# Optimization experiments

Measured on AMD Instinct MI355X. Metric: run time of the kernel, lower is better.

## Reference

```python
import jax, jax.numpy as jnp
import numpy as np
import math

B, N, C = 16, 4096, 256
WS = 8            # window_size
NH = 8            # num_heads
HD = C // NH      # head_dim = 32
LK = 32           # linformer compressed length
G = 16            # global bank tokens


def setup_inputs() -> dict:
    key = jax.random.key(0)
    ks = jax.random.split(key, 10)
    x = jax.random.normal(ks[0], (B, N, C), dtype=jnp.float32)
    W_qkv = jax.random.normal(ks[1], (C, 3 * C), dtype=jnp.float32) * 0.02
    b_qkv = jnp.zeros((3 * C,), dtype=jnp.float32)
    E_k = jax.random.normal(ks[2], (WS * WS, LK), dtype=jnp.float32) * 0.02
    E_v = jax.random.normal(ks[3], (WS * WS, LK), dtype=jnp.float32) * 0.02
    k_bank = jax.random.normal(ks[4], (G, C), dtype=jnp.float32)
    v_bank = jax.random.normal(ks[5], (G, C), dtype=jnp.float32)
    W_proj = jax.random.normal(ks[6], (C, C), dtype=jnp.float32) * 0.02
    b_proj = jnp.zeros((C,), dtype=jnp.float32)
    return {"x": x, "W_qkv": W_qkv, "b_qkv": b_qkv, "E_k": E_k, "E_v": E_v,
            "k_bank": k_bank, "v_bank": v_bank, "W_proj": W_proj, "b_proj": b_proj,
            "window_size": WS, "num_heads": NH}


def reference(x, W_qkv, b_qkv, E_k, E_v, k_bank, v_bank, W_proj, b_proj, window_size, num_heads):
    Bb, Nn, Cc = x.shape
    Hs = int(math.isqrt(Nn))          # H = W = sqrt(N), divisible by window_size here
    ws = window_size
    nh = Hs // ws                      # windows per side
    hd = Cc // num_heads
    NW = ws * ws                       # tokens per window

    # ---- window partition: [B,N,C] -> [BW, NW, C]
    xw = x.reshape(Bb, nh, ws, nh, ws, Cc).transpose(0, 1, 3, 2, 4, 5)
    xw = xw.reshape(Bb * nh * nh, NW, Cc)
    BW = xw.shape[0]

    # ---- qkv projection and head split: (3, BW, H, NW, hd)
    qkv = (xw @ W_qkv + b_qkv).reshape(BW, NW, 3, num_heads, hd)
    qkv = qkv.transpose(2, 0, 3, 1, 4)
    q, k, v = qkv[0], qkv[1], qkv[2]

    # ---- Linformer KV compression: NW == seq_len (no pad branch)
    k_c = jnp.einsum('nk,bhnd->bhkd', E_k, k)   # [BW,H,LK,hd]
    v_c = jnp.einsum('nk,bhnd->bhkd', E_v, v)

    # ---- global memory bank, broadcast to all windows: [BW,H,G,hd]
    Gt = k_bank.shape[0]
    kb = jnp.broadcast_to(k_bank.reshape(Gt, num_heads, hd).transpose(1, 0, 2)[None],
                          (BW, num_heads, Gt, hd))
    vb = jnp.broadcast_to(v_bank.reshape(Gt, num_heads, hd).transpose(1, 0, 2)[None],
                          (BW, num_heads, Gt, hd))

    k_full = jnp.concatenate([k_c, kb], axis=2)  # [BW,H,LK+G,hd]
    v_full = jnp.concatenate([v_c, vb], axis=2)

    # ---- SDPA (dropout_p = 0)
    scale = 1.0 / math.sqrt(hd)
    scores = jnp.einsum('bhqd,bhkd->bhqk', q, k_full) * scale
    attn = jax.nn.softmax(scores, axis=-1)
    out = jnp.einsum('bhqk,bhkd->bhqd', attn, v_full)     # [BW,H,NW,hd]

    out = out.transpose(0, 2, 1, 3).reshape(BW, NW, Cc)
    out = out @ W_proj + b_proj

    # ---- window reverse: [BW,NW,C] -> [B,N,C]
    out = out.reshape(Bb, nh, nh, ws, ws, Cc).transpose(0, 1, 3, 2, 4, 5)
    out = out.reshape(Bb, Hs * Hs, Cc)
    return out
```

## Files before the change

### kernel.cpp

```cpp
#include <hip/hip_runtime.h>
#include <hip/hip_bf16.h>


typedef unsigned int uint;
typedef __attribute__((ext_vector_type(8))) short short8;
typedef __attribute__((ext_vector_type(4))) float f32x4;

__device__ __forceinline__ float bup(uint hs) {
    return __uint_as_float(hs << 16);
}
__device__ __forceinline__ uint f2b(float f) {
    __hip_bfloat16 h = __float2bfloat16(f);
    unsigned short u;
    __builtin_memcpy(&u, &h, 2);
    return (uint)u;
}
__device__ __forceinline__ uint f2b2(float a, float b) {
    __hip_bfloat162 h = __float22bfloat162_rn(make_float2(a, b));
    uint u;
    __builtin_memcpy(&u, &h, 4);
    return u;
}
__device__ __forceinline__ f32x4 mfma16(short8 a, short8 b, f32x4 c) {
    return __builtin_amdgcn_mfma_f32_16x16x32_bf16(a, b, c, 0, 0, 0);
}
__device__ __forceinline__ int sw256(int r, int c) { return r * 256 + (c ^ ((r & 7) << 3)); }
__device__ __forceinline__ int sw64 (int r, int c) { return r * 64  + (c ^ ((r & 7) << 3)); }
__device__ __forceinline__ int sw32 (int r, int c) { return r * 32  + (c ^ ((r & 3) << 3)); }

#define WS_WHQ 0
#define WS_WHP 196608
#define WS_WLP 262144
#define WS_EKT 327680
#define WS_EVT 329728

__global__ void __launch_bounds__(256)
eswa_prep(const float* __restrict__ Wqkv, const float* __restrict__ Wproj,
          const float* __restrict__ Ek, const float* __restrict__ Ev,
          short* __restrict__ wsp)
{
    const int blk = blockIdx.x, thr = threadIdx.x;
    if (blk < 192) {
        const int jh = blk & 1;
        const int g = (blk >> 1) * 256 + thr;
        const int lane = g & 63, tk = (g >> 6) & 7, tn = g >> 9;
        const int quad = lane >> 4, l16 = lane & 15;
        const int c = tn * 16 + l16;
        const int r0 = tk * 32 + quad * 8 + jh * 4;
        const float w0 = Wqkv[(r0 + 0) * 768 + c], w1 = Wqkv[(r0 + 1) * 768 + c];
        const float w2 = Wqkv[(r0 + 2) * 768 + c], w3 = Wqkv[(r0 + 3) * 768 + c];
        *(uint2*)(wsp + WS_WHQ + ((tn * 8 + tk) * 64 + lane) * 8 + jh * 4) =
            make_uint2(f2b2(w0, w1), f2b2(w2, w3));
    } else if (blk < 256) {
        const int idx = blk - 192, jh = idx & 1;
        const int g = (idx >> 1) * 256 + thr;
        const int lane = g & 63, tk = (g >> 6) & 7, tn = g >> 9;
        const int quad = lane >> 4, l16 = lane & 15;
        const int c = tn * 16 + l16;
        const int r0 = tk * 32 + quad * 8 + jh * 4;
        float w[4];
        #pragma unroll
        for (int j = 0; j < 4; ++j) w[j] = Wproj[(r0 + j) * 256 + c];
        const uint h01 = f2b2(w[0], w[1]), h23 = f2b2(w[2], w[3]);
        const float l0 = w[0] - bup(h01 & 0xffffu), l1 = w[1] - bup(h01 >> 16);
        const float l2 = w[2] - bup(h23 & 0xffffu), l3 = w[3] - bup(h23 >> 16);
        const int o = ((tn * 8 + tk) * 64 + lane) * 8 + jh * 4;
        *(uint2*)(wsp + WS_WHP + o) = make_uint2(h01, h23);
        *(uint2*)(wsp + WS_WLP + o) = make_uint2(f2b2(l0, l1), f2b2(l2, l3));
    } else {
        const float* E = (blk == 256) ? Ek : Ev;
        const int base = (blk == 256) ? WS_EKT : WS_EVT;
        const int lane = thr & 63, tk = (thr >> 6) & 1, tm = (thr >> 7) & 1;
        const int quad = lane >> 4, l16 = lane & 15;
        const int lk = tm * 16 + l16;
        uint pk[4];
        #pragma unroll
        for (int jp = 0; jp < 4; ++jp) {
            const int t = tk * 32 + quad * 8 + jp * 2;
            pk[jp] = f2b2(E[t * 32 + lk], E[(t + 1) * 32 + lk]);
        }
        *(uint4*)(wsp + base + ((tm * 2 + tk) * 64 + lane) * 8) =
            make_uint4(pk[0], pk[1], pk[2], pk[3]);
    }
}

#define SMEM_BYTES 131072

__global__ void __launch_bounds__(1024, 4)
eswa_main(const float* __restrict__ x, const float* __restrict__ bqkv,
          const float* __restrict__ kbank, const float* __restrict__ vbank,
          const float* __restrict__ bproj, const short* __restrict__ wsp,
          float* __restrict__ out)
{
    extern __shared__ char smem[];
    short* xh = (short*)smem;

    const int tid  = threadIdx.x;
    const int wave = tid >> 6;
    const int lane = tid & 63;
    const int quad = lane >> 4;
    const int l16  = lane & 15;

    const int b  = blockIdx.x >> 6;
    const int w  = blockIdx.x & 63;
    const int rw = w >> 3;
    const int cw = w & 7;

    #pragma unroll
    for (int i = 0; i < 4; ++i) {
        const int vi = tid + 1024 * i;
        const int t  = vi >> 6;
        const int c  = (vi & 63) * 4;
        const int n  = (rw * 8 + (t >> 3)) * 64 + cw * 8 + (t & 7);
        const float4 xv = *(const float4*)(x + (size_t)(b * 4096 + n) * 256 + c);
        *(uint2*)(xh + sw256(t, c)) = make_uint2(f2b2(xv.x, xv.y), f2b2(xv.z, xv.w));
    }
    __syncthreads();

    {
        const short* Whq = wsp + WS_WHQ;
        const int tn0 = wave * 3;
        f32x4 acc[3][4];
        #pragma unroll
        for (int p = 0; p < 3; ++p) {
            const int tn = tn0 + p;
            const int sec = tn >> 4, hh = (tn >> 1) & 7, half = tn & 1;
            const float bv = bqkv[sec * 256 + hh * 32 + half * 16 + l16];
            #pragma unroll
            for (int m = 0; m < 4; ++m) acc[p][m] = (f32x4){bv, bv, bv, bv};
        }
        #pragma unroll 2
        for (int tk = 0; tk < 8; ++tk) {
            short8 af[4];
            #pragma unroll
            for (int m = 0; m < 4; ++m)
                af[m] = *(const short8*)(xh + sw256(m * 16 + l16, tk * 32 + quad * 8));
            #pragma unroll
            for (int p = 0; p < 3; ++p) {
                const short8 bh = *(const short8*)(Whq + (((tn0 + p) * 8 + tk) * 64 + lane) * 8);
                #pragma unroll
                for (int m = 0; m < 4; ++m)
                    acc[p][m] = mfma16(af[m], bh, acc[p][m]);
            }
        }
        #pragma unroll
        for (int p = 0; p < 3; ++p) {
            const int tn = tn0 + p;
            const int sec = tn >> 4, hh = (tn >> 1) & 7, half = tn & 1;
            short* arena = (short*)(smem + 32768 + hh * 12288);
            #pragma unroll
            for (int m = 0; m < 4; ++m) {
                #pragma unroll
                for (int r = 0; r < 4; ++r) {
                    const int t = m * 16 + quad * 4 + r;
                    const float v = acc[p][m][r];
                    if (sec == 0)
                        arena[sw32(t, half * 16 + l16)] =
                            (short)f2b(v * 0.17677669529663687f);
                    else if (sec == 1)
                        (arena + 2048)[sw64(half * 16 + l16, t)] = (short)f2b(v);
                    else
                        (arena + 4096)[sw64(half * 16 + l16, t)] = (short)f2b(v);
                }
            }
        }
    }
    __syncthreads();

    const int h = wave >> 1, s = wave & 1;
    short* arena = (short*)(smem + 32768 + h * 12288);
    short* qsp = arena;
    short* kTp = arena + 2048;
    short* vTp = arena + 4096;
    const int gB  = s * 8 + (lane >> 3);
    const int dqB = (lane & 7) * 4;

    short8 kB[2][2], vB[2][2];
    #pragma unroll
    for (int tn = 0; tn < 2; ++tn)
        #pragma unroll
        for (int tk = 0; tk < 2; ++tk) {
            kB[tn][tk] = *(const short8*)(kTp + sw64(tn * 16 + l16, tk * 32 + quad * 8));
            vB[tn][tk] = *(const short8*)(vTp + sw64(tn * 16 + l16, tk * 32 + quad * 8));
        }
    short8 akE[2], avE[2];
    #pragma unroll
    for (int tk = 0; tk < 2; ++tk) {
        akE[tk] = *(const short8*)(wsp + WS_EKT + ((s * 2 + tk) * 64 + lane) * 8);
        avE[tk] = *(const short8*)(wsp + WS_EVT + ((s * 2 + tk) * 64 + lane) * 8);
    }
    const float4 kbv = *(const float4*)(kbank + gB * 256 + h * 32 + dqB);
    const float4 vbv = *(const float4*)(vbank + gB * 256 + h * 32 + dqB);
    __syncthreads();

    {
        f32x4 kc[2], vc[2];
        #pragma unroll
        for (int tn = 0; tn < 2; ++tn) { kc[tn] = (f32x4){0,0,0,0}; vc[tn] = (f32x4){0,0,0,0}; }
        #pragma unroll
        for (int tk = 0; tk < 2; ++tk)
            #pragma unroll
            for (int tn = 0; tn < 2; ++tn) {
                kc[tn] = mfma16(akE[tk], kB[tn][tk], kc[tn]);
                vc[tn] = mfma16(avE[tk], vB[tn][tk], vc[tn]);
            }
        #pragma unroll
        for (int tn = 0; tn < 2; ++tn)
            #pragma unroll
            for (int r = 0; r < 4; ++r) {
                const int lk = s * 16 + quad * 4 + r;
                const int d  = tn * 16 + l16;
                kTp[sw32(lk, d)] = (short)f2b(kc[tn][r]);
                vTp[sw64(d, lk)] = (short)f2b(vc[tn][r]);
            }
        *(uint2*)(kTp + sw32(32 + gB, dqB)) =
            make_uint2(f2b2(kbv.x, kbv.y), f2b2(kbv.z, kbv.w));
        vTp[sw64(dqB + 0, 32 + gB)] = (short)f2b(vbv.x);
        vTp[sw64(dqB + 1, 32 + gB)] = (short)f2b(vbv.y);
        vTp[sw64(dqB + 2, 32 + gB)] = (short)f2b(vbv.z);
        vTp[sw64(dqB + 3, 32 + gB)] = (short)f2b(vbv.w);
        if (s == 0)
            *(uint4*)(vTp + sw64(lane >> 1, 48 + (lane & 1) * 8)) = make_uint4(0, 0, 0, 0);
    }
    __syncthreads();

    f32x4 sc[2][3];
    f32x4 inv4[2];
    {
        short8 qA[2], kfB[3];
        #pragma unroll
        for (int ml = 0; ml < 2; ++ml)
            qA[ml] = *(const short8*)(qsp + sw32((2 * s + ml) * 16 + l16, quad * 8));
        #pragma unroll
        for (int n = 0; n < 3; ++n)
            kfB[n] = *(const short8*)(kTp + sw32(n * 16 + l16, quad * 8));
        #pragma unroll
        for (int ml = 0; ml < 2; ++ml)
            #pragma unroll
            for (int n = 0; n < 3; ++n) {
                sc[ml][n] = (f32x4){0, 0, 0, 0};
                sc[ml][n] = mfma16(qA[ml], kfB[n], sc[ml][n]);
            }
        #pragma unroll
        for (int ml = 0; ml < 2; ++ml) {
            #pragma unroll
            for (int r = 0; r < 4; ++r) {
                float mm = fmaxf(fmaxf(sc[ml][0][r], sc[ml][1][r]), sc[ml][2][r]);
                mm = fmaxf(mm, __shfl_xor(mm, 1));
                mm = fmaxf(mm, __shfl_xor(mm, 2));
                mm = fmaxf(mm, __shfl_xor(mm, 4));
                mm = fmaxf(mm, __shfl_xor(mm, 8));
                const float e0 = __expf(sc[ml][0][r] - mm);
                const float e1 = __expf(sc[ml][1][r] - mm);
                const float e2 = __expf(sc[ml][2][r] - mm);
                sc[ml][0][r] = e0; sc[ml][1][r] = e1; sc[ml][2][r] = e2;
                float su = e0 + e1 + e2;
                su += __shfl_xor(su, 1);
                su += __shfl_xor(su, 2);
                su += __shfl_xor(su, 4);
                su += __shfl_xor(su, 8);
                inv4[ml][r] = 1.0f / su;
            }
        }
    }
    __syncthreads();

    {
        short* Pb = (s == 0) ? qsp : kTp;
        #pragma unroll
        for (int ml = 0; ml < 2; ++ml)
            #pragma unroll
            for (int n = 0; n < 3; ++n)
                #pragma unroll
                for (int r = 0; r < 4; ++r)
                    Pb[sw64(ml * 16 + quad * 4 + r, n * 16 + l16)] =
                        (short)f2b(sc[ml][n][r] * inv4[ml][r]);
        *(uint4*)(Pb + sw64(lane >> 1, 48 + (lane & 1) * 8)) = make_uint4(0, 0, 0, 0);

        short8 vfB[2][2], pA[2][2];
        #pragma unroll
        for (int tn = 0; tn < 2; ++tn)
            #pragma unroll
            for (int tk = 0; tk < 2; ++tk)
                vfB[tn][tk] = *(const short8*)(vTp + sw64(tn * 16 + l16, tk * 32 + quad * 8));
        #pragma unroll
        for (int ml = 0; ml < 2; ++ml)
            #pragma unroll
            for (int tk = 0; tk < 2; ++tk)
                pA[ml][tk] = *(const short8*)(Pb + sw64(ml * 16 + l16, tk * 32 + quad * 8));
        #pragma unroll
        for (int ml = 0; ml < 2; ++ml)
            #pragma unroll
            for (int tn = 0; tn < 2; ++tn) {
                f32x4 oa = (f32x4){0, 0, 0, 0};
                oa = mfma16(pA[ml][0], vfB[tn][0], oa);
                oa = mfma16(pA[ml][1], vfB[tn][1], oa);
                #pragma unroll
                for (int r = 0; r < 4; ++r) {
                    const int t = s * 32 + ml * 16 + quad * 4 + r;
                    ((short*)smem)[sw256(t, h * 32 + tn * 16 + l16)] =
                        (short)f2b(oa[r]);
                }
            }
    }
    __syncthreads();

    {
        const short* Whp = wsp + WS_WHP;
        const short* Wlp = wsp + WS_WLP;
        const short* attnS = (const short*)smem;
        const int tn = wave;
        f32x4 acc[4];
        {
            const float bi = bproj[tn * 16 + l16];
            #pragma unroll
            for (int m = 0; m < 4; ++m) acc[m] = (f32x4){bi, bi, bi, bi};
        }
        #pragma unroll 2
        for (int tk = 0; tk < 8; ++tk) {
            short8 aA[4];
            #pragma unroll
            for (int m = 0; m < 4; ++m)
                aA[m] = *(const short8*)(attnS + sw256(m * 16 + l16, tk * 32 + quad * 8));
            const int bo = ((tn * 8 + tk) * 64 + lane) * 8;
            const short8 bh = *(const short8*)(Whp + bo);
            const short8 bl = *(const short8*)(Wlp + bo);
            #pragma unroll
            for (int m = 0; m < 4; ++m) {
                acc[m] = mfma16(aA[m], bh, acc[m]);
                acc[m] = mfma16(aA[m], bl, acc[m]);
            }
        }
        #pragma unroll
        for (int m = 0; m < 4; ++m)
            #pragma unroll
            for (int r = 0; r < 4; ++r) {
                const int t = m * 16 + quad * 4 + r;
                const int n = (rw * 8 + (t >> 3)) * 64 + cw * 8 + (t & 7);
                out[(size_t)(b * 4096 + n) * 256 + tn * 16 + l16] = acc[m][r];
            }
    }
}

extern "C" void kernel_launch(void* const* d_in, const int* in_sizes, int n_in,
                              void* d_out, int out_size, void* d_ws, size_t ws_size,
                              hipStream_t stream) {
    const float* x     = (const float*)d_in[0];
    const float* Wqkv  = (const float*)d_in[1];
    const float* bqkv  = (const float*)d_in[2];
    const float* Ek    = (const float*)d_in[3];
    const float* Ev    = (const float*)d_in[4];
    const float* kbank = (const float*)d_in[5];
    const float* vbank = (const float*)d_in[6];
    const float* Wproj = (const float*)d_in[7];
    const float* bproj = (const float*)d_in[8];
    float* outp        = (float*)d_out;
    short* wsp         = (short*)d_ws;
    (void)in_sizes; (void)n_in; (void)out_size; (void)ws_size;

    hipFuncSetAttribute((const void*)eswa_main,
                        hipFuncAttributeMaxDynamicSharedMemorySize, SMEM_BYTES);

    eswa_prep<<<258, 256, 0, stream>>>(Wqkv, Wproj, Ek, Ev, wsp);
    eswa_main<<<1024, 1024, SMEM_BYTES, stream>>>(x, bqkv, kbank, vbank, bproj,
                                                  wsp, outp);
}
```

Measured before the change: 208.7 us.

## Keep per-head QKV and attention in registers via shuffle transposes, halve block size

Each wave now owns one head and computes its own K, V and Q projections, keeping them in registers. Lane-shuffle transposes replace the per-head shared-memory arenas and the extra block barriers between stages. Bank K/V fragments are pre-packed in the prep kernel. The block shrinks to 512 threads and 64KB of shared memory so more blocks can be resident. The trade-off is more register pressure and shuffle instructions, and each wave now does a larger share of the output projection.

Result: faster. 187.8 us (-10.0%).

```diff
diff --git a/kernel.cpp b/kernel.cpp
--- a/kernel.cpp
+++ b/kernel.cpp
@@ -5,6 +5,7 @@
 typedef unsigned int uint;
 typedef __attribute__((ext_vector_type(8))) short short8;
 typedef __attribute__((ext_vector_type(4))) float f32x4;
+typedef __attribute__((ext_vector_type(4))) uint uintx4;
 
 __device__ __forceinline__ float bup(uint hs) {
     return __uint_as_float(hs << 16);
@@ -25,18 +26,39 @@
     return __builtin_amdgcn_mfma_f32_16x16x32_bf16(a, b, c, 0, 0, 0);
 }
 __device__ __forceinline__ int sw256(int r, int c) { return r * 256 + (c ^ ((r & 7) << 3)); }
-__device__ __forceinline__ int sw64 (int r, int c) { return r * 64  + (c ^ ((r & 7) << 3)); }
-__device__ __forceinline__ int sw32 (int r, int c) { return r * 32  + (c ^ ((r & 3) << 3)); }
+
+__device__ __forceinline__ short8 xpose(f32x4 a, f32x4 b, float s, int lane) {
+    const uint pa0 = f2b2(a[0] * s, a[1] * s), pa1 = f2b2(a[2] * s, a[3] * s);
+    const uint pb0 = f2b2(b[0] * s, b[1] * s), pb1 = f2b2(b[2] * s, b[3] * s);
+    const int s0 = ((lane >> 4) & 1) * 32 + (lane & 15);
+    const int s1 = s0 + 16;
+    const uint w0a = __shfl(pa0, s0), w0b = __shfl(pb0, s0);
+    const uint w1a = __shfl(pa1, s0), w1b = __shfl(pb1, s0);
+    const uint w2a = __shfl(pa0, s1), w2b = __shfl(pb0, s1);
+    const uint w3a = __shfl(pa1, s1), w3b = __shfl(pb1, s1);
+    const bool hi = lane >= 32;
+    uintx4 u;
+    u[0] = hi ? w0b : w0a;
+    u[1] = hi ? w1b : w1a;
+    u[2] = hi ? w2b : w2a;
+    u[3] = hi ? w3b : w3a;
+    short8 r;
+    __builtin_memcpy(&r, &u, 16);
+    return r;
+}
 
 #define WS_WHQ 0
 #define WS_WHP 196608
 #define WS_WLP 262144
 #define WS_EKT 327680
 #define WS_EVT 329728
+#define WS_KBF 331776
+#define WS_VBF 335872
 
 __global__ void __launch_bounds__(256)
 eswa_prep(const float* __restrict__ Wqkv, const float* __restrict__ Wproj,
           const float* __restrict__ Ek, const float* __restrict__ Ev,
+          const float* __restrict__ kbank, const float* __restrict__ vbank,
           short* __restrict__ wsp)
 {
     const int blk = blockIdx.x, thr = threadIdx.x;
@@ -67,7 +89,7 @@
         const int o = ((tn * 8 + tk) * 64 + lane) * 8 + jh * 4;
         *(uint2*)(wsp + WS_WHP + o) = make_uint2(h01, h23);
         *(uint2*)(wsp + WS_WLP + o) = make_uint2(f2b2(l0, l1), f2b2(l2, l3));
-    } else {
+    } else if (blk < 258) {
         const float* E = (blk == 256) ? Ek : Ev;
         const int base = (blk == 256) ? WS_EKT : WS_EVT;
         const int lane = thr & 63, tk = (thr >> 6) & 1, tm = (thr >> 7) & 1;
@@ -81,25 +103,49 @@
         }
         *(uint4*)(wsp + base + ((tm * 2 + tk) * 64 + lane) * 8) =
             make_uint4(pk[0], pk[1], pk[2], pk[3]);
-    }
-}
-
-#define SMEM_BYTES 131072
-
-__global__ void __launch_bounds__(1024, 4)
+    } else {
+        for (int idx = thr; idx < 512; idx += 256) {
+            const int hh = idx >> 6, l = idx & 63;
+            const int l16 = l & 15, q = l >> 4;
+            uint pk[4];
+            #pragma unroll
+            for (int jp = 0; jp < 4; ++jp)
+                pk[jp] = f2b2(kbank[l16 * 256 + hh * 32 + q * 8 + jp * 2],
+                              kbank[l16 * 256 + hh * 32 + q * 8 + jp * 2 + 1]);
+            *(uint4*)(wsp + WS_KBF + idx * 8) = make_uint4(pk[0], pk[1], pk[2], pk[3]);
+        }
+        for (int idx = thr; idx < 1024; idx += 256) {
+            const int hh = idx >> 7, md = (idx >> 6) & 1, l = idx & 63;
+            const int l16 = l & 15, q = l >> 4;
+            uint pk[4] = {0u, 0u, 0u, 0u};
+            if (q < 2) {
+                #pragma unroll
+                for (int jp = 0; jp < 4; ++jp)
+                    pk[jp] = f2b2(vbank[(q * 8 + jp * 2) * 256 + hh * 32 + md * 16 + l16],
+                                  vbank[(q * 8 + jp * 2 + 1) * 256 + hh * 32 + md * 16 + l16]);
+            }
+            *(uint4*)(wsp + WS_VBF + idx * 8) = make_uint4(pk[0], pk[1], pk[2], pk[3]);
+        }
+    }
+}
+
+#define SMEM_BYTES 65536
+
+__global__ void __launch_bounds__(512, 4)
 eswa_main(const float* __restrict__ x, const float* __restrict__ bqkv,
-          const float* __restrict__ kbank, const float* __restrict__ vbank,
           const float* __restrict__ bproj, const short* __restrict__ wsp,
           float* __restrict__ out)
 {
     extern __shared__ char smem[];
-    short* xh = (short*)smem;
+    short* xh   = (short*)smem;
+    short* attn = (short*)smem + 16384;
 
     const int tid  = threadIdx.x;
     const int wave = tid >> 6;
     const int lane = tid & 63;
     const int quad = lane >> 4;
     const int l16  = lane & 15;
+    const int h    = wave;
 
     const int b  = blockIdx.x >> 6;
     const int w  = blockIdx.x & 63;
@@ -107,8 +153,8 @@
     const int cw = w & 7;
 
     #pragma unroll
-    for (int i = 0; i < 4; ++i) {
-        const int vi = tid + 1024 * i;
+    for (int i = 0; i < 8; ++i) {
+        const int vi = tid + 512 * i;
         const int t  = vi >> 6;
         const int c  = (vi & 63) * 4;
         const int n  = (rw * 8 + (t >> 3)) * 64 + cw * 8 + (t & 7);
@@ -117,190 +163,207 @@
     }
     __syncthreads();
 
+    const short* WF = wsp + WS_WHQ;
+
+    short8 kfr[2][2], vfr[2][2];
     {
-        const short* Whq = wsp + WS_WHQ;
-        const int tn0 = wave * 3;
-        f32x4 acc[3][4];
-        #pragma unroll
-        for (int p = 0; p < 3; ++p) {
-            const int tn = tn0 + p;
-            const int sec = tn >> 4, hh = (tn >> 1) & 7, half = tn & 1;
-            const float bv = bqkv[sec * 256 + hh * 32 + half * 16 + l16];
-            #pragma unroll
-            for (int m = 0; m < 4; ++m) acc[p][m] = (f32x4){bv, bv, bv, bv};
+        f32x4 acc[2][4];
+        #pragma unroll
+        for (int nd = 0; nd < 2; ++nd) {
+            const float bk = bqkv[256 + h * 32 + nd * 16 + l16];
+            #pragma unroll
+            for (int mt = 0; mt < 4; ++mt) acc[nd][mt] = (f32x4){bk, bk, bk, bk};
         }
         #pragma unroll 2
         for (int tk = 0; tk < 8; ++tk) {
-            short8 af[4];
-            #pragma unroll
-            for (int m = 0; m < 4; ++m)
-                af[m] = *(const short8*)(xh + sw256(m * 16 + l16, tk * 32 + quad * 8));
-            #pragma unroll
-            for (int p = 0; p < 3; ++p) {
-                const short8 bh = *(const short8*)(Whq + (((tn0 + p) * 8 + tk) * 64 + lane) * 8);
-                #pragma unroll
-                for (int m = 0; m < 4; ++m)
-                    acc[p][m] = mfma16(af[m], bh, acc[p][m]);
-            }
-        }
-        #pragma unroll
-        for (int p = 0; p < 3; ++p) {
-            const int tn = tn0 + p;
-            const int sec = tn >> 4, hh = (tn >> 1) & 7, half = tn & 1;
-            short* arena = (short*)(smem + 32768 + hh * 12288);
-            #pragma unroll
-            for (int m = 0; m < 4; ++m) {
-                #pragma unroll
-                for (int r = 0; r < 4; ++r) {
-                    const int t = m * 16 + quad * 4 + r;
-                    const float v = acc[p][m][r];
-                    if (sec == 0)
-                        arena[sw32(t, half * 16 + l16)] =
-                            (short)f2b(v * 0.17677669529663687f);
-                    else if (sec == 1)
-                        (arena + 2048)[sw64(half * 16 + l16, t)] = (short)f2b(v);
-                    else
-                        (arena + 4096)[sw64(half * 16 + l16, t)] = (short)f2b(v);
-                }
-            }
-        }
+            short8 xf[4];
+            #pragma unroll
+            for (int mt = 0; mt < 4; ++mt)
+                xf[mt] = *(const short8*)(xh + sw256(mt * 16 + l16, tk * 32 + quad * 8));
+            #pragma unroll
+            for (int nd = 0; nd < 2; ++nd) {
+                const short8 wf =
+                    *(const short8*)(WF + (((16 + h * 2 + nd) * 8 + tk) * 64 + lane) * 8);
+                #pragma unroll
+                for (int mt = 0; mt < 4; ++mt) acc[nd][mt] = mfma16(xf[mt], wf, acc[nd][mt]);
+            }
+        }
+        #pragma unroll
+        for (int nd = 0; nd < 2; ++nd)
+            #pragma unroll
+            for (int kk = 0; kk < 2; ++kk)
+                kfr[nd][kk] = xpose(acc[nd][2 * kk], acc[nd][2 * kk + 1], 1.0f, lane);
+    }
+    {
+        f32x4 acc[2][4];
+        #pragma unroll
+        for (int nd = 0; nd < 2; ++nd) {
+            const float bv = bqkv[512 + h * 32 + nd * 16 + l16];
+            #pragma unroll
+            for (int mt = 0; mt < 4; ++mt) acc[nd][mt] = (f32x4){bv, bv, bv, bv};
+        }
+        #pragma unroll 2
+        for (int tk = 0; tk < 8; ++tk) {
+            short8 xf[4];
+            #pragma unroll
+            for (int mt = 0; mt < 4; ++mt)
+                xf[mt] = *(const short8*)(xh + sw256(mt * 16 + l16, tk * 32 + quad * 8));
+            #pragma unroll
+            for (int nd = 0; nd < 2; ++nd) {
+                const short8 wf =
+                    *(const short8*)(WF + (((32 + h * 2 + nd) * 8 + tk) * 64 + lane) * 8);
+                #pragma unroll
+                for (int mt = 0; mt < 4; ++mt) acc[nd][mt] = mfma16(xf[mt], wf, acc[nd][mt]);
+            }
+        }
+        #pragma unroll
+        for (int nd = 0; nd < 2; ++nd)
+            #pragma unroll
+            for (int kk = 0; kk < 2; ++kk)
+                vfr[nd][kk] = xpose(acc[nd][2 * kk], acc[nd][2 * kk + 1], 1.0f, lane);
+    }
+    short8 kcf[2], vcf[2];
+    {
+        short8 ekf[2][2], evf[2][2];
+        #pragma unroll
+        for (int tm = 0; tm < 2; ++tm)
+            #pragma unroll
+            for (int kk = 0; kk < 2; ++kk) {
+                ekf[tm][kk] = *(const short8*)(wsp + WS_EKT + ((tm * 2 + kk) * 64 + lane) * 8);
+                evf[tm][kk] = *(const short8*)(wsp + WS_EVT + ((tm * 2 + kk) * 64 + lane) * 8);
+            }
+        f32x4 ck[2][2];
+        #pragma unroll
+        for (int md = 0; md < 2; ++md)
+            #pragma unroll
+            for (int nl = 0; nl < 2; ++nl) ck[md][nl] = (f32x4){0, 0, 0, 0};
+        #pragma unroll
+        for (int kk = 0; kk < 2; ++kk)
+            #pragma unroll
+            for (int md = 0; md < 2; ++md)
+                #pragma unroll
+                for (int nl = 0; nl < 2; ++nl)
+                    ck[md][nl] = mfma16(kfr[md][kk], ekf[nl][kk], ck[md][nl]);
+        #pragma unroll
+        for (int nl = 0; nl < 2; ++nl)
+            kcf[nl] = xpose(ck[0][nl], ck[1][nl], 1.0f, lane);
+        f32x4 cv[2][2];
+        #pragma unroll
+        for (int ml = 0; ml < 2; ++ml)
+            #pragma unroll
+            for (int nd = 0; nd < 2; ++nd) cv[ml][nd] = (f32x4){0, 0, 0, 0};
+        #pragma unroll
+        for (int kk = 0; kk < 2; ++kk)
+            #pragma unroll
+            for (int ml = 0; ml < 2; ++ml)
+                #pragma unroll
+                for (int nd = 0; nd < 2; ++nd)
+                    cv[ml][nd] = mfma16(evf[ml][kk], vfr[nd][kk], cv[ml][nd]);
+        #pragma unroll
+        for (int nd = 0; nd < 2; ++nd)
+            vcf[nd] = xpose(cv[0][nd], cv[1][nd], 1.0f, lane);
+    }
+    const short8 kbf = *(const short8*)(wsp + WS_KBF + (h * 64 + lane) * 8);
+    short8 vbf[2];
+    #pragma unroll
+    for (int md = 0; md < 2; ++md)
+        vbf[md] = *(const short8*)(wsp + WS_VBF + ((h * 2 + md) * 64 + lane) * 8);
+
+    short8 qfr[4];
+    {
+        f32x4 acc[2][4];
+        #pragma unroll
+        for (int md = 0; md < 2; ++md) {
+            const float4 bq = *(const float4*)(bqkv + h * 32 + md * 16 + quad * 4);
+            #pragma unroll
+            for (int nt = 0; nt < 4; ++nt) acc[md][nt] = (f32x4){bq.x, bq.y, bq.z, bq.w};
+        }
+        #pragma unroll 2
+        for (int tk = 0; tk < 8; ++tk) {
+            short8 xf[4];
+            #pragma unroll
+            for (int nt = 0; nt < 4; ++nt)
+                xf[nt] = *(const short8*)(xh + sw256(nt * 16 + l16, tk * 32 + quad * 8));
+            #pragma unroll
+            for (int md = 0; md < 2; ++md) {
+                const short8 wf =
+                    *(const short8*)(WF + (((h * 2 + md) * 8 + tk) * 64 + lane) * 8);
+                #pragma unroll
+                for (int nt = 0; nt < 4; ++nt) acc[md][nt] = mfma16(wf, xf[nt], acc[md][nt]);
+            }
+        }
+        #pragma unroll
+        for (int nt = 0; nt < 4; ++nt)
+            qfr[nt] = xpose(acc[0][nt], acc[1][nt], 0.17677669529663687f, lane);
     }
     __syncthreads();
 
-    const int h = wave >> 1, s = wave & 1;
-    short* arena = (short*)(smem + 32768 + h * 12288);
-    short* qsp = arena;
-    short* kTp = arena + 2048;
-    short* vTp = arena + 4096;
-    const int gB  = s * 8 + (lane >> 3);
-    const int dqB = (lane & 7) * 4;
-
-    short8 kB[2][2], vB[2][2];
+    short* scr = (short*)smem + wave * 2048;
+    if (lane >= 32) {
+        *(uint4*)(scr + (1 * 64 + lane) * 8) = make_uint4(0, 0, 0, 0);
+        *(uint4*)(scr + (3 * 64 + lane) * 8) = make_uint4(0, 0, 0, 0);
+    }
+
     #pragma unroll
-    for (int tn = 0; tn < 2; ++tn)
-        #pragma unroll
-        for (int tk = 0; tk < 2; ++tk) {
-            kB[tn][tk] = *(const short8*)(kTp + sw64(tn * 16 + l16, tk * 32 + quad * 8));
-            vB[tn][tk] = *(const short8*)(vTp + sw64(tn * 16 + l16, tk * 32 + quad * 8));
-        }
-    short8 akE[2], avE[2];
-    #pragma unroll
-    for (int tk = 0; tk < 2; ++tk) {
-        akE[tk] = *(const short8*)(wsp + WS_EKT + ((s * 2 + tk) * 64 + lane) * 8);
-        avE[tk] = *(const short8*)(wsp + WS_EVT + ((s * 2 + tk) * 64 + lane) * 8);
-    }
-    const float4 kbv = *(const float4*)(kbank + gB * 256 + h * 32 + dqB);
-    const float4 vbv = *(const float4*)(vbank + gB * 256 + h * 32 + dqB);
-    __syncthreads();
-
-    {
-        f32x4 kc[2], vc[2];
-        #pragma unroll
-        for (int tn = 0; tn < 2; ++tn) { kc[tn] = (f32x4){0,0,0,0}; vc[tn] = (f32x4){0,0,0,0}; }
-        #pragma unroll
-        for (int tk = 0; tk < 2; ++tk)
-            #pragma unroll
-            for (int tn = 0; tn < 2; ++tn) {
-                kc[tn] = mfma16(akE[tk], kB[tn][tk], kc[tn]);
-                vc[tn] = mfma16(avE[tk], vB[tn][tk], vc[tn]);
-            }
-        #pragma unroll
-        for (int tn = 0; tn < 2; ++tn)
+    for (int th = 0; th < 2; ++th) {
+        f32x4 sc[2][3];
+        #pragma unroll
+        for (int mt = 0; mt < 2; ++mt) {
+            const short8 qa = qfr[th * 2 + mt];
+            sc[mt][0] = mfma16(qa, kcf[0], (f32x4){0, 0, 0, 0});
+            sc[mt][1] = mfma16(qa, kcf[1], (f32x4){0, 0, 0, 0});
+            sc[mt][2] = mfma16(qa, kbf,    (f32x4){0, 0, 0, 0});
+        }
+        float inv[2][4];
+        #pragma unroll
+        for (int mt = 0; mt < 2; ++mt) {
             #pragma unroll
             for (int r = 0; r < 4; ++r) {
-                const int lk = s * 16 + quad * 4 + r;
-                const int d  = tn * 16 + l16;
-                kTp[sw32(lk, d)] = (short)f2b(kc[tn][r]);
-                vTp[sw64(d, lk)] = (short)f2b(vc[tn][r]);
-            }
-        *(uint2*)(kTp + sw32(32 + gB, dqB)) =
-            make_uint2(f2b2(kbv.x, kbv.y), f2b2(kbv.z, kbv.w));
-        vTp[sw64(dqB + 0, 32 + gB)] = (short)f2b(vbv.x);
-        vTp[sw64(dqB + 1, 32 + gB)] = (short)f2b(vbv.y);
-        vTp[sw64(dqB + 2, 32 + gB)] = (short)f2b(vbv.z);
-        vTp[sw64(dqB + 3, 32 + gB)] = (short)f2b(vbv.w);
-        if (s == 0)
-            *(uint4*)(vTp + sw64(lane >> 1, 48 + (lane & 1) * 8)) = make_uint4(0, 0, 0, 0);
-    }
-    __syncthreads();
-
-    f32x4 sc[2][3];
-    f32x4 inv4[2];
-    {
-        short8 qA[2], kfB[3];
-        #pragma unroll
-        for (int ml = 0; ml < 2; ++ml)
-            qA[ml] = *(const short8*)(qsp + sw32((2 * s + ml) * 16 + l16, quad * 8));
-        #pragma unroll
-        for (int n = 0; n < 3; ++n)
-            kfB[n] = *(const short8*)(kTp + sw32(n * 16 + l16, quad * 8));
-        #pragma unroll
-        for (int ml = 0; ml < 2; ++ml)
-            #pragma unroll
-            for (int n = 0; n < 3; ++n) {
-                sc[ml][n] = (f32x4){0, 0, 0, 0};
-                sc[ml][n] = mfma16(qA[ml], kfB[n], sc[ml][n]);
-            }
-        #pragma unroll
-        for (int ml = 0; ml < 2; ++ml) {
-            #pragma unroll
-            for (int r = 0; r < 4; ++r) {
-                float mm = fmaxf(fmaxf(sc[ml][0][r], sc[ml][1][r]), sc[ml][2][r]);
+                float mm = fmaxf(fmaxf(sc[mt][0][r], sc[mt][1][r]), sc[mt][2][r]);
                 mm = fmaxf(mm, __shfl_xor(mm, 1));
                 mm = fmaxf(mm, __shfl_xor(mm, 2));
                 mm = fmaxf(mm, __shfl_xor(mm, 4));
                 mm = fmaxf(mm, __shfl_xor(mm, 8));
-                const float e0 = __expf(sc[ml][0][r] - mm);
-                const float e1 = __expf(sc[ml][1][r] - mm);
-                const float e2 = __expf(sc[ml][2][r] - mm);
-                sc[ml][0][r] = e0; sc[ml][1][r] = e1; sc[ml][2][r] = e2;
+                const float e0 = __expf(sc[mt][0][r] - mm);
+                const float e1 = __expf(sc[mt][1][r] - mm);
+                const float e2 = __expf(sc[mt][2][r] - mm);
+                sc[mt][0][r] = e0; sc[mt][1][r] = e1; sc[mt][2][r] = e2;
                 float su = e0 + e1 + e2;
                 su += __shfl_xor(su, 1);
                 su += __shfl_xor(su, 2);
                 su += __shfl_xor(su, 4);
                 su += __shfl_xor(su, 8);
-                inv4[ml][r] = 1.0f / su;
-            }
-        }
-    }
-    __syncthreads();
-
-    {
-        short* Pb = (s == 0) ? qsp : kTp;
-        #pragma unroll
-        for (int ml = 0; ml < 2; ++ml)
-            #pragma unroll
-            for (int n = 0; n < 3; ++n)
+                inv[mt][r] = 1.0f / su;
+            }
+        }
+        #pragma unroll
+        for (int mt = 0; mt < 2; ++mt)
+            #pragma unroll
+            for (int nk = 0; nk < 3; ++nk) {
+                const int qt = (nk * 2 + (l16 >> 3)) & 3;
+                const int base = (mt * 2 + (nk >> 1)) * 64 + qt * 16 + quad * 4;
                 #pragma unroll
                 for (int r = 0; r < 4; ++r)
-                    Pb[sw64(ml * 16 + quad * 4 + r, n * 16 + l16)] =
-                        (short)f2b(sc[ml][n][r] * inv4[ml][r]);
-        *(uint4*)(Pb + sw64(lane >> 1, 48 + (lane & 1) * 8)) = make_uint4(0, 0, 0, 0);
-
-        short8 vfB[2][2], pA[2][2];
-        #pragma unroll
-        for (int tn = 0; tn < 2; ++tn)
-            #pragma unroll
-            for (int tk = 0; tk < 2; ++tk)
-                vfB[tn][tk] = *(const short8*)(vTp + sw64(tn * 16 + l16, tk * 32 + quad * 8));
-        #pragma unroll
-        for (int ml = 0; ml < 2; ++ml)
-            #pragma unroll
-            for (int tk = 0; tk < 2; ++tk)
-                pA[ml][tk] = *(const short8*)(Pb + sw64(ml * 16 + l16, tk * 32 + quad * 8));
-        #pragma unroll
-        for (int ml = 0; ml < 2; ++ml)
-            #pragma unroll
-            for (int tn = 0; tn < 2; ++tn) {
-                f32x4 oa = (f32x4){0, 0, 0, 0};
-                oa = mfma16(pA[ml][0], vfB[tn][0], oa);
-                oa = mfma16(pA[ml][1], vfB[tn][1], oa);
-                #pragma unroll
-                for (int r = 0; r < 4; ++r) {
-                    const int t = s * 32 + ml * 16 + quad * 4 + r;
-                    ((short*)smem)[sw256(t, h * 32 + tn * 16 + l16)] =
-                        (short)f2b(oa[r]);
-                }
+                    scr[(base + r) * 8 + (l16 & 7)] =
+                        (short)f2b(sc[mt][nk][r] * inv[mt][r]);
+            }
+        asm volatile("s_waitcnt lgkmcnt(0)" ::: "memory");
+        __builtin_amdgcn_sched_barrier(0);
+        short8 pa[2][2];
+        #pragma unroll
+        for (int mt = 0; mt < 2; ++mt)
+            #pragma unroll
+            for (int kk = 0; kk < 2; ++kk)
+                pa[mt][kk] = *(const short8*)(scr + ((mt * 2 + kk) * 64 + lane) * 8);
+        #pragma unroll
+        for (int mt = 0; mt < 2; ++mt)
+            #pragma unroll
+            for (int md = 0; md < 2; ++md) {
+                f32x4 o = mfma16(vcf[md], pa[mt][0], (f32x4){0, 0, 0, 0});
+                o = mfma16(vbf[md], pa[mt][1], o);
+                *(uint2*)(attn + sw256((th * 2 + mt) * 16 + l16,
+                                       h * 32 + md * 16 + quad * 4)) =
+                    make_uint2(f2b2(o[0], o[1]), f2b2(o[2], o[3]));
             }
     }
     __syncthreads();
@@ -308,37 +371,42 @@
     {
         const short* Whp = wsp + WS_WHP;
         const short* Wlp = wsp + WS_WLP;
-        const short* attnS = (const short*)smem;
-        const int tn = wave;
-        f32x4 acc[4];
-        {
-            const float bi = bproj[tn * 16 + l16];
-            #pragma unroll
-            for (int m = 0; m < 4; ++m) acc[m] = (f32x4){bi, bi, bi, bi};
+        f32x4 acc[2][4];
+        #pragma unroll
+        for (int p = 0; p < 2; ++p) {
+            const float bi = bproj[(wave * 2 + p) * 16 + l16];
+            #pragma unroll
+            for (int m = 0; m < 4; ++m) acc[p][m] = (f32x4){bi, bi, bi, bi};
         }
         #pragma unroll 2
         for (int tk = 0; tk < 8; ++tk) {
             short8 aA[4];
             #pragma unroll
             for (int m = 0; m < 4; ++m)
-                aA[m] = *(const short8*)(attnS + sw256(m * 16 + l16, tk * 32 + quad * 8));
-            const int bo = ((tn * 8 + tk) * 64 + lane) * 8;
-            const short8 bh = *(const short8*)(Whp + bo);
-            const short8 bl = *(const short8*)(Wlp + bo);
-            #pragma unroll
-            for (int m = 0; m < 4; ++m) {
-                acc[m] = mfma16(aA[m], bh, acc[m]);
-                acc[m] = mfma16(aA[m], bl, acc[m]);
-            }
-        }
-        #pragma unroll
-        for (int m = 0; m < 4; ++m)
-            #pragma unroll
-            for (int r = 0; r < 4; ++r) {
-                const int t = m * 16 + quad * 4 + r;
-                const int n = (rw * 8 + (t >> 3)) * 64 + cw * 8 + (t & 7);
-                out[(size_t)(b * 4096 + n) * 256 + tn * 16 + l16] = acc[m][r];
-            }
+                aA[m] = *(const short8*)(attn + sw256(m * 16 + l16, tk * 32 + quad * 8));
+            #pragma unroll
+            for (int p = 0; p < 2; ++p) {
+                const int bo = (((wave * 2 + p) * 8 + tk) * 64 + lane) * 8;
+                const short8 bh = *(const short8*)(Whp + bo);
+                const short8 bl = *(const short8*)(Wlp + bo);
+                #pragma unroll
+                for (int m = 0; m < 4; ++m) {
+                    acc[p][m] = mfma16(aA[m], bh, acc[p][m]);
+                    acc[p][m] = mfma16(aA[m], bl, acc[p][m]);
+                }
+            }
+        }
+        #pragma unroll
+        for (int p = 0; p < 2; ++p)
+            #pragma unroll
+            for (int m = 0; m < 4; ++m)
+                #pragma unroll
+                for (int r = 0; r < 4; ++r) {
+                    const int t = m * 16 + quad * 4 + r;
+                    const int n = (rw * 8 + (t >> 3)) * 64 + cw * 8 + (t & 7);
+                    out[(size_t)(b * 4096 + n) * 256 + (wave * 2 + p) * 16 + l16] =
+                        acc[p][m][r];
+                }
     }
 }
 
@@ -358,10 +426,9 @@
     short* wsp         = (short*)d_ws;
     (void)in_sizes; (void)n_in; (void)out_size; (void)ws_size;
 
-    hipFuncSetAttribute((const void*)eswa_main,
-                        hipFuncAttributeMaxDynamicSharedMemorySize, SMEM_BYTES);
-
-    eswa_prep<<<258, 256, 0, stream>>>(Wqkv, Wproj, Ek, Ev, wsp);
-    eswa_main<<<1024, 1024, SMEM_BYTES, stream>>>(x, bqkv, kbank, vbank, bproj,
-                                                  wsp, outp);
-}
+    (void)hipFuncSetAttribute((const void*)eswa_main,
+                              hipFuncAttributeMaxDynamicSharedMemorySize, SMEM_BYTES);
+
+    eswa_prep<<<259, 256, 0, stream>>>(Wqkv, Wproj, Ek, Ev, kbank, vbank, wsp);
+    eswa_main<<<1024, 512, SMEM_BYTES, stream>>>(x, bqkv, bproj, wsp, outp);
+}
```
